# Performance work log

Hardware: AMD Instinct MI355X
Metric: run time of the kernel (lower is better)

Reference implementation:

```python
import jax, jax.numpy as jnp
import numpy as np

N = 20000      # num nodes
E = 320000     # num edges
F_IN = 512
HEADS = 8
D = 64         # out_features per head (512 / 8)
ALPHA = 0.2    # leaky relu slope
EPS = 1e-16


def setup_inputs() -> dict:
    key = jax.random.key(0)
    k1, k2, k3, k4, k5 = jax.random.split(key, 5)
    x = jax.random.normal(k1, (N, F_IN), dtype=jnp.float32)
    edge_index = jax.random.randint(k2, (2, E), 0, N, dtype=jnp.int64)
    # per-head parameters (xavier-normal-ish scale)
    s_w = np.sqrt(2.0 / (F_IN + D))
    W_e = jax.random.normal(k3, (HEADS, F_IN, D), dtype=jnp.float32) * s_w
    W_r = jax.random.normal(k4, (HEADS, F_IN, D), dtype=jnp.float32) * s_w
    # attention vector over concat of [h_src, h_dst, diff, |diff|, prod] -> 5*D
    s_a = np.sqrt(2.0 / (1 + 5 * D))
    a = jax.random.normal(k5, (HEADS, 5 * D), dtype=jnp.float32) * s_a
    return {"x": x, "edge_index": edge_index, "W_e": W_e, "W_r": W_r, "a": a}


def _gat_forward(x, edge_index, W_e, W_r, a):
    src = edge_index[0]  # [E] softmax / output rows
    dst = edge_index[1]  # [E]

    h_e = jnp.einsum('nf,hfd->hnd', x, W_e)  # [H,N,D]
    h_r = jnp.einsum('nf,hfd->hnd', x, W_r)  # [H,N,D]

    a_src, a_dst, a_dif, a_abs, a_prd = jnp.split(a, 5, axis=1)  # each [H,D]

    # node-level dot products for the linear concat parts, then gather
    s_src = jnp.einsum('hnd,hd->hn', h_e, a_src)[:, src]  # [H,E]
    s_dst = jnp.einsum('hnd,hd->hn', h_e, a_dst)[:, dst]  # [H,E]

    hr_src = h_r[:, src]            # [H,E,D]
    hr_dst = h_r[:, dst]            # [H,E,D]
    diff = hr_dst - hr_src          # [H,E,D]
    score = (s_src + s_dst
             + jnp.einsum('hed,hd->he', diff, a_dif)
             + jnp.einsum('hed,hd->he', jnp.abs(diff), a_abs)
             + jnp.einsum('hed,hd->he', hr_src * hr_dst, a_prd))  # [H,E]

    alpha = jax.nn.leaky_relu(score, negative_slope=ALPHA)  # [H,E]

    # sparse softmax over edges grouped by source node
    alpha_t = alpha.T  # [E,H]
    m = jax.ops.segment_max(alpha_t, src, num_segments=N)        # [N,H]
    ex = jnp.exp(alpha_t - m[src])                                # [E,H]
    denom = jax.ops.segment_sum(ex, src, num_segments=N)[src]    # [E,H]
    att = ex / (denom + EPS)                                      # [E,H]

    # spmm: out[src] += att * h_e[dst]
    msg = att[:, :, None] * jnp.transpose(h_e[:, dst], (1, 0, 2))  # [E,H,D]
    out = jax.ops.segment_sum(msg, src, num_segments=N)            # [N,H,D]
    return out.reshape(N, HEADS * D)  # concat heads along feature dim


def reference(x, edge_index, W_e, W_r, a):
    return _gat_forward(x, edge_index, W_e, W_r, a)
```

## Files before the change

### kernel.cpp

```cpp
#include <hip/hip_runtime.h>
#include <hip/hip_bf16.h>

#define N_NODES 20000
#define N_EDGES 320000
#define F_IN 512
#define HEADS 8
#define DH 64
#define KPAD 64

typedef _Float16 f16;
typedef __attribute__((ext_vector_type(8))) _Float16 half8;
typedef __attribute__((ext_vector_type(4))) _Float16 half4v;
typedef __attribute__((ext_vector_type(2))) _Float16 half2v;
typedef __attribute__((ext_vector_type(4))) float f32x4;

__device__ __forceinline__ void async_copy16(void* lds_base, const void* g) {
  __builtin_amdgcn_global_load_lds(
      (const __attribute__((address_space(1))) unsigned int*)g,
      (__attribute__((address_space(3))) unsigned int*)lds_base, 16, 0, 0);
}

#define CX_BLOCKS 10000
#define CW_BLOCKS 128
#define SCAT_BLOCKS 1250

__global__ __launch_bounds__(256) void prologue_kernel(
    const float* __restrict__ x, const float* __restrict__ We,
    const float* __restrict__ Wr, const int* __restrict__ ei,
    f16* __restrict__ xh, f16* __restrict__ Wt,
    int* __restrict__ cnt, int* __restrict__ csr)
{
  __shared__ f16 tile[64 * 65];
  const int b = blockIdx.x;
  if (b < CX_BLOCKS) {
    int i = (b * 256 + threadIdx.x) * 4;
    float4 v = *(const float4*)&x[i];
    half4v o;
    o[0] = (f16)v.x; o[1] = (f16)v.y; o[2] = (f16)v.z; o[3] = (f16)v.w;
    *(half4v*)&xh[i] = o;
  } else if (b < CX_BLOCKS + CW_BLOCKS) {
    const int bb = b - CX_BLOCKS;
    const int kt = (bb & 7) * 64;
    const int h = (bb >> 3) & 7;
    const int mat = bb >> 6;
    const float* __restrict__ W = (mat ? Wr : We) + (size_t)h * F_IN * DH;
    #pragma unroll
    for (int r = 0; r < 16; ++r) {
      int idx = r * 256 + threadIdx.x;
      int k = idx >> 6, d = idx & 63;
      tile[d * 65 + k] = (f16)W[(size_t)(kt + k) * DH + d];
    }
    __syncthreads();
    f16* __restrict__ Wo = Wt + (size_t)(mat * 8 + h) * 64 * F_IN;
    #pragma unroll
    for (int r = 0; r < 16; ++r) {
      int idx = r * 256 + threadIdx.x;
      int d = idx >> 6, k = idx & 63;
      Wo[(size_t)d * F_IN + kt + k] = tile[d * 65 + k];
    }
  } else {
    int e = (b - CX_BLOCKS - CW_BLOCKS) * 256 + threadIdx.x;
    if (e < N_EDGES) {
      int s = ei[e];
      int t = ei[N_EDGES + e];
      int pos = atomicAdd(&cnt[s], 1);
      if (pos < KPAD) csr[s * KPAD + pos] = t;
    }
  }
}

#define GBM 128
#define GBN 128
#define GBK 64
#define MT_TOTAL 157
#define MT_PER_GRP 20
#define NKT (F_IN / GBK)

__global__ __launch_bounds__(256) void gemm_mfma(
    const f16* __restrict__ xh, const f16* __restrict__ Wt,
    f16* __restrict__ hef, const float* __restrict__ a,
    float* __restrict__ ssrc, float* __restrict__ sdst)
{
  const int b = blockIdx.x;
  const int g = b & 7;
  const int j = b >> 3;
  const int m_tile = g * MT_PER_GRP + (j >> 3);
  const int c_tile = j & 7;
  if (m_tile >= MT_TOTAL) return;

  __shared__ f16 As[2][GBM * GBK];
  __shared__ f16 Bs[2][GBN * GBK];
  const int tid = threadIdx.x;
  const int m0 = m_tile * GBM;
  const int n0 = c_tile * GBN;
  const int wv = tid >> 6, lane = tid & 63, quad = lane >> 4, l16 = lane & 15;
  const int wm = (wv >> 1) * 64;
  const int wn = (wv & 1) * 64;
  const int lrow = lane >> 3;
  const int gc = (lane & 7) ^ (lrow & 7);

  f32x4 acc[4][4] = {};

  auto stage = [&](int kt, int buf) {
    #pragma unroll
    for (int s = 0; s < 4; ++s) {
      int seg = wv * 4 + s;
      int row = seg * 8 + lrow;
      async_copy16(&As[buf][seg * 512],
                   &xh[(size_t)(m0 + row) * F_IN + kt + gc * 8]);
      async_copy16(&Bs[buf][seg * 512],
                   &Wt[(size_t)(n0 + row) * F_IN + kt + gc * 8]);
    }
  };

  stage(0, 0);
  __syncthreads();
  for (int it = 0; it < NKT; ++it) {
    if (it + 1 < NKT) stage((it + 1) * GBK, (it + 1) & 1);
    const f16* __restrict__ Ab = &As[it & 1][0];
    const f16* __restrict__ Bb = &Bs[it & 1][0];
    #pragma unroll
    for (int ks = 0; ks < 2; ++ks) {
      half8 af[4], bf4[4];
      const int ch = ((ks << 2) + quad) ^ (l16 & 7);
      #pragma unroll
      for (int i = 0; i < 4; ++i)
        af[i] = *(const half8*)&Ab[(wm + i * 16 + l16) * GBK + ch * 8];
      #pragma unroll
      for (int jj = 0; jj < 4; ++jj)
        bf4[jj] = *(const half8*)&Bb[(wn + jj * 16 + l16) * GBK + ch * 8];
      #pragma unroll
      for (int i = 0; i < 4; ++i)
        #pragma unroll
        for (int jj = 0; jj < 4; ++jj)
          acc[i][jj] = __builtin_amdgcn_mfma_f32_16x16x32_f16(af[i], bf4[jj], acc[i][jj], 0, 0, 0);
    }
    __syncthreads();
  }

  const int cb = c_tile * 2 + (wv & 1);
  const int mat = cb >> 3, h = cb & 7;
  #pragma unroll
  for (int i = 0; i < 4; ++i) {
    #pragma unroll
    for (int r = 0; r < 4; ++r) {
      int m = m0 + wm + i * 16 + quad * 4 + r;
      if (m < N_NODES) {
        #pragma unroll
        for (int jj = 0; jj < 4; ++jj)
          hef[(size_t)m * 1024 + mat * 512 + h * DH + jj * 16 + l16] = (f16)acc[i][jj][r];
      }
    }
  }

  if (mat == 0) {
    float as4[4], ad4[4];
    #pragma unroll
    for (int jj = 0; jj < 4; ++jj) {
      as4[jj] = a[h * 320 + jj * 16 + l16];
      ad4[jj] = a[h * 320 + 64 + jj * 16 + l16];
    }
    #pragma unroll
    for (int i = 0; i < 4; ++i) {
      #pragma unroll
      for (int r = 0; r < 4; ++r) {
        int m = m0 + wm + i * 16 + quad * 4 + r;
        float v1 = 0.f, v2 = 0.f;
        #pragma unroll
        for (int jj = 0; jj < 4; ++jj) {
          v1 = fmaf(acc[i][jj][r], as4[jj], v1);
          v2 = fmaf(acc[i][jj][r], ad4[jj], v2);
        }
        #pragma unroll
        for (int s = 1; s < 16; s <<= 1) {
          v1 += __shfl_xor(v1, s);
          v2 += __shfl_xor(v2, s);
        }
        if (l16 == 0 && m < N_NODES) {
          ssrc[(size_t)m * HEADS + h] = v1;
          sdst[(size_t)m * HEADS + h] = v2;
        }
      }
    }
  }
}

__global__ __launch_bounds__(256) void attn_kernel(
    const f16* __restrict__ hef, const float* __restrict__ a,
    const float* __restrict__ ssrc, const float* __restrict__ sdst,
    const int* __restrict__ cnt, const int* __restrict__ csr,
    float* __restrict__ out)
{
  const int wv = threadIdx.x >> 6;
  const int n = blockIdx.x * 4 + wv;
  const int lane = threadIdx.x & 63;
  const int h = lane >> 3;
  const int d0 = (lane & 7) * 8;
  const int deg = min(cnt[n], KPAD);
  const int beg = n * KPAD, end = beg + deg;

  const half8 hrn = *(const half8*)&hef[(size_t)n * 1024 + lane * 8 + 512];
  half2v adif2[4], aabs2[4], aprd2[4];
  const int ab = h * 320;
  #pragma unroll
  for (int c = 0; c < 4; ++c) {
    adif2[c][0] = (f16)a[ab + 128 + d0 + 2 * c];
    adif2[c][1] = (f16)a[ab + 128 + d0 + 2 * c + 1];
    aabs2[c][0] = (f16)a[ab + 192 + d0 + 2 * c];
    aabs2[c][1] = (f16)a[ab + 192 + d0 + 2 * c + 1];
    aprd2[c][0] = (f16)a[ab + 256 + d0 + 2 * c];
    aprd2[c][1] = (f16)a[ab + 256 + d0 + 2 * c + 1];
  }
  const float sbase = ssrc[(size_t)n * HEADS + h];

  float denom = 0.f;
  float acc[8] = {};

  auto edge = [&](half8 he8, half8 hr8, float sd) {
    half8 df = hr8 - hrn;
    uint4 u = __builtin_bit_cast(uint4, df);
    u.x &= 0x7FFF7FFFu; u.y &= 0x7FFF7FFFu; u.z &= 0x7FFF7FFFu; u.w &= 0x7FFF7FFFu;
    half8 ad = __builtin_bit_cast(half8, u);
    half8 pr = hr8 * hrn;
    float v = 0.f;
    #pragma unroll
    for (int c = 0; c < 4; ++c) {
      half2v df2 = {df[2 * c], df[2 * c + 1]};
      half2v ad2 = {ad[2 * c], ad[2 * c + 1]};
      half2v pr2 = {pr[2 * c], pr[2 * c + 1]};
      v = __builtin_amdgcn_fdot2(df2, adif2[c], v, false);
      v = __builtin_amdgcn_fdot2(ad2, aabs2[c], v, false);
      v = __builtin_amdgcn_fdot2(pr2, aprd2[c], v, false);
    }
    v += __shfl_xor(v, 1);
    v += __shfl_xor(v, 2);
    v += __shfl_xor(v, 4);
    float sc = sbase + sd + v;
    sc = fmaxf(sc, 0.2f * sc);
    float ex = __expf(sc);
    denom += ex;
    #pragma unroll
    for (int jj = 0; jj < 8; ++jj) acc[jj] = fmaf(ex, (float)he8[jj], acc[jj]);
  };

  int i = beg;
  for (; i + 2 <= end; i += 2) {
    int t0 = csr[i], t1 = csr[i + 1];
    size_t b0 = (size_t)t0 * 1024 + lane * 8;
    size_t b1 = (size_t)t1 * 1024 + lane * 8;
    half8 e0 = *(const half8*)&hef[b0];
    half8 r0 = *(const half8*)&hef[b0 + 512];
    half8 e1 = *(const half8*)&hef[b1];
    half8 r1 = *(const half8*)&hef[b1 + 512];
    float s0 = sdst[(size_t)t0 * HEADS + h];
    float s1 = sdst[(size_t)t1 * HEADS + h];
    edge(e0, r0, s0);
    edge(e1, r1, s1);
  }
  if (i < end) {
    int t = csr[i];
    size_t b0 = (size_t)t * 1024 + lane * 8;
    half8 e0 = *(const half8*)&hef[b0];
    half8 r0 = *(const half8*)&hef[b0 + 512];
    edge(e0, r0, sdst[(size_t)t * HEADS + h]);
  }

  float inv = 1.f / (denom + 1e-16f);
  float4 o0, o1;
  o0.x = acc[0] * inv; o0.y = acc[1] * inv; o0.z = acc[2] * inv; o0.w = acc[3] * inv;
  o1.x = acc[4] * inv; o1.y = acc[5] * inv; o1.z = acc[6] * inv; o1.w = acc[7] * inv;
  *(float4*)&out[(size_t)n * 512 + lane * 8] = o0;
  *(float4*)&out[(size_t)n * 512 + lane * 8 + 4] = o1;
}

extern "C" void kernel_launch(void* const* d_in, const int* in_sizes, int n_in,
                              void* d_out, int out_size, void* d_ws, size_t ws_size,
                              hipStream_t stream) {
  const float* x  = (const float*)d_in[0];
  const int*   ei = (const int*)d_in[1];
  const float* We = (const float*)d_in[2];
  const float* Wr = (const float*)d_in[3];
  const float* a  = (const float*)d_in[4];
  float* out = (float*)d_out;

  char* ws = (char*)d_ws;
  size_t p = 0;
  auto alloc = [&](size_t bytes) {
    void* r = ws + p;
    p = (p + bytes + 255) & ~(size_t)255;
    return r;
  };
  f16* xh  = (f16*)alloc(sizeof(f16) * (size_t)N_NODES * F_IN);
  f16* Wt  = (f16*)alloc(sizeof(f16) * 2 * HEADS * F_IN * DH);
  f16* hef = (f16*)alloc(sizeof(f16) * (size_t)N_NODES * 1024);
  float* ssrc = (float*)alloc(sizeof(float) * (size_t)N_NODES * HEADS);
  float* sdst = (float*)alloc(sizeof(float) * (size_t)N_NODES * HEADS);
  int* cnt = (int*)alloc(sizeof(int) * N_NODES);
  int* csr = (int*)alloc(sizeof(int) * (size_t)N_NODES * KPAD);

  hipMemsetAsync(cnt, 0, sizeof(int) * N_NODES, stream);

  prologue_kernel<<<CX_BLOCKS + CW_BLOCKS + SCAT_BLOCKS, 256, 0, stream>>>(
      x, We, Wr, ei, xh, Wt, cnt, csr);

  gemm_mfma<<<8 * MT_PER_GRP * 8, 256, 0, stream>>>(xh, Wt, hef, a, ssrc, sdst);

  attn_kernel<<<N_NODES / 4, 256, 0, stream>>>(hef, a, ssrc, sdst, cnt, csr, out);
}
```

Baseline: 249.9 us.

## Prefetch neighbor rows three edges ahead using lane-broadcast CSR indices

The attention kernel now loads all of a node's CSR neighbor indices in one coalesced per-lane read, and broadcasts each index with readlane. The edge loop becomes a three-deep software pipeline: the gathers for the next edges are issued while the current ones are computed. This is meant to hide the latency of the random hef and sdst gathers. In exchange, the edge count is padded up to a multiple of three, using dummy edges whose score is -1e30 so their exp is zero, and register pressure rises from the six buffered half8 vectors.

Measured after the change: 251.2 us. No clear change (+0.5%).

```diff
diff --git a/kernel.cpp b/kernel.cpp
--- a/kernel.cpp
+++ b/kernel.cpp
@@ -197,7 +197,10 @@
   const int h = lane >> 3;
   const int d0 = (lane & 7) * 8;
   const int deg = min(cnt[n], KPAD);
-  const int beg = n * KPAD, end = beg + deg;
+  const int beg = n * KPAD;
+
+  int myT = csr[beg + lane];
+  if (lane >= deg) myT = n;
 
   const half8 hrn = *(const half8*)&hef[(size_t)n * 1024 + lane * 8 + 512];
   half2v adif2[4], aabs2[4], aprd2[4];
@@ -216,7 +219,7 @@
   float denom = 0.f;
   float acc[8] = {};
 
-  auto edge = [&](half8 he8, half8 hr8, float sd) {
+  auto cmp = [&](half8 he8, half8 hr8, float sd) {
     half8 df = hr8 - hrn;
     uint4 u = __builtin_bit_cast(uint4, df);
     u.x &= 0x7FFF7FFFu; u.y &= 0x7FFF7FFFu; u.z &= 0x7FFF7FFFu; u.w &= 0x7FFF7FFFu;
@@ -243,27 +246,34 @@
     for (int jj = 0; jj < 8; ++jj) acc[jj] = fmaf(ex, (float)he8[jj], acc[jj]);
   };
 
-  int i = beg;
-  for (; i + 2 <= end; i += 2) {
-    int t0 = csr[i], t1 = csr[i + 1];
-    size_t b0 = (size_t)t0 * 1024 + lane * 8;
-    size_t b1 = (size_t)t1 * 1024 + lane * 8;
-    half8 e0 = *(const half8*)&hef[b0];
-    half8 r0 = *(const half8*)&hef[b0 + 512];
-    half8 e1 = *(const half8*)&hef[b1];
-    half8 r1 = *(const half8*)&hef[b1 + 512];
-    float s0 = sdst[(size_t)t0 * HEADS + h];
-    float s1 = sdst[(size_t)t1 * HEADS + h];
-    edge(e0, r0, s0);
-    edge(e1, r1, s1);
-  }
-  if (i < end) {
-    int t = csr[i];
-    size_t b0 = (size_t)t * 1024 + lane * 8;
-    half8 e0 = *(const half8*)&hef[b0];
-    half8 r0 = *(const half8*)&hef[b0 + 512];
-    edge(e0, r0, sdst[(size_t)t * HEADS + h]);
-  }
+  half8 E0, E1, E2, R0, R1, R2;
+  float S0, S1, S2;
+
+#define PRE(K, J) {                                                      \
+    int t = __builtin_amdgcn_readlane(myT, (J));                         \
+    t = (t < 0) ? 0 : ((t >= N_NODES) ? (N_NODES - 1) : t);              \
+    const f16* p = &hef[(size_t)t * 1024 + lane * 8];                    \
+    E##K = *(const half8*)p;                                             \
+    R##K = *(const half8*)&p[512];                                       \
+    float sv = sdst[(size_t)t * HEADS + h];                              \
+    S##K = ((J) < deg) ? sv : -1e30f;                                    \
+  }
+
+  const int iters = (deg + 2) / 3;
+
+  PRE(0, 0)
+  PRE(1, 1)
+  PRE(2, 2)
+  for (int g = 1; g < iters; ++g) {
+    const int j3 = g * 3;
+    cmp(E0, R0, S0); PRE(0, j3)
+    cmp(E1, R1, S1); PRE(1, j3 + 1)
+    cmp(E2, R2, S2); PRE(2, j3 + 2)
+  }
+  cmp(E0, R0, S0);
+  cmp(E1, R1, S1);
+  cmp(E2, R2, S2);
+#undef PRE
 
   float inv = 1.f / (denom + 1e-16f);
   float4 o0, o1;
```
